# Optimization experiments

Measured on AMD Instinct MI355X. Metric: run time of the kernel, lower is better.

The kernel has to match this reference:

```python
import jax, jax.numpy as jnp
import numpy as np

B, N, K = 4, 4096, 16
C_IN = 128
EPS = 1e-5


def setup_inputs() -> dict:
    key = jax.random.key(0)
    ks = jax.random.split(key, 8)
    c0 = 2 * C_IN + 3  # concat channels: pos_diff(3) + feat2(128) + feat1(128)
    return {
        "pos1": jax.random.normal(ks[0], (B, 3, N), jnp.float32),
        "pos2": jax.random.normal(ks[1], (B, 3, N), jnp.float32),
        "feature1": jax.random.normal(ks[2], (B, C_IN, N), jnp.float32),
        "feature2": jax.random.normal(ks[3], (B, C_IN, N), jnp.float32),
        "W0": jax.random.normal(ks[4], (128, c0), jnp.float32) * 0.05,
        "W1": jax.random.normal(ks[5], (128, 128), jnp.float32) * 0.05,
        "W2": jax.random.normal(ks[6], (128, 128), jnp.float32) * 0.05,
        "g0": jnp.ones((128,), jnp.float32),
        "g1": jnp.ones((128,), jnp.float32),
        "g2": jnp.ones((128,), jnp.float32),
        "b0": jnp.zeros((128,), jnp.float32),
        "b1": jnp.zeros((128,), jnp.float32),
        "b2": jnp.zeros((128,), jnp.float32),
    }


def _knn_idx(pos1, pos2, k):
    # pos1, pos2: (B, 3, N).  For each point in pos1, k nearest points in pos2.
    p1 = pos1.transpose(0, 2, 1)  # (B, N, 3)
    p2 = pos2.transpose(0, 2, 1)  # (B, M, 3)
    d = (jnp.sum(p1 * p1, -1, keepdims=True)
         + jnp.sum(p2 * p2, -1)[:, None, :]
         - 2.0 * jnp.einsum("bnc,bmc->bnm", p1, p2))  # (B, N, M) squared dists
    _, idx = jax.lax.top_k(-d, k)  # (B, N, K)
    return idx


def _group(x, idx):
    # x: (B, C, M), idx: (B, N, K) -> (B, C, N, K)
    xt = x.transpose(0, 2, 1)  # (B, M, C)
    g = jax.vmap(lambda a, i: a[i])(xt, idx)  # (B, N, K, C)
    return g.transpose(0, 3, 1, 2)


def _conv_bn_relu(x, W, g, b):
    # 1x1 conv (no bias) + BatchNorm2d (training: batch stats, biased var) + ReLU
    y = jnp.einsum("oc,bcnk->bonk", W, x)
    mu = jnp.mean(y, axis=(0, 2, 3), keepdims=True)
    var = jnp.var(y, axis=(0, 2, 3), keepdims=True)
    yn = (y - mu) * jax.lax.rsqrt(var + EPS)
    return jax.nn.relu(yn * g[None, :, None, None] + b[None, :, None, None])


def reference(pos1, pos2, feature1, feature2, W0, W1, W2, g0, g1, g2, b0, b1, b2):
    idx = _knn_idx(pos1, pos2, K)                      # (B, N, K)
    pos2_g = _group(pos2, idx)                         # (B, 3, N, K)
    pos_diff = pos2_g - pos1[:, :, :, None]
    feat2_g = _group(feature2, idx)                    # (B, C, N, K)
    feat1_rep = jnp.broadcast_to(feature1[:, :, :, None], (B, C_IN, N, K))
    x = jnp.concatenate([pos_diff, feat2_g, feat1_rep], axis=1)  # (B, 2C+3, N, K)
    x = _conv_bn_relu(x, W0, g0, b0)
    x = _conv_bn_relu(x, W1, g1, b1)
    x = _conv_bn_relu(x, W2, g2, b2)
    feat1_new = jnp.max(x, axis=-1)                    # (B, mlp[-1], N)
    return (pos1, feat1_new)
```

## Files before the change

kernel.cpp:

```cpp
#include <hip/hip_runtime.h>

#define B_ 4
#define N_ 4096
#define K_ 16
#define C_ 128
#define NQ (B_*N_)
#define COLS_TOT (NQ*K_)
#define CNT_F 262144.0f
#define EPS_ 1e-5f

typedef __attribute__((ext_vector_type(8))) short short8;
typedef __attribute__((ext_vector_type(4))) float f4;
typedef __attribute__((ext_vector_type(4))) int i4;

__device__ __forceinline__ unsigned short f2bf(float f){
  unsigned u = __builtin_bit_cast(unsigned, f);
  u = u + 0x7fffu + ((u >> 16) & 1u);
  return (unsigned short)(u >> 16);
}
__device__ __forceinline__ float bf2f(unsigned short h){
  return __builtin_bit_cast(float, ((unsigned)h) << 16);
}
__device__ __forceinline__ int swzc(int c){ return c ^ ((c >> 3) & 7); }

__global__ __launch_bounds__(256) void wconv(
    const float* __restrict__ W0, const float* __restrict__ W1, const float* __restrict__ W2,
    unsigned short* __restrict__ W0b, unsigned short* __restrict__ W0c,
    unsigned short* __restrict__ W1b, unsigned short* __restrict__ W2b)
{
  int i = blockIdx.x * 256 + threadIdx.x;
  int sel = i >> 14, r = i & 16383;
  int o = r >> 7, c = r & 127;
  float v; unsigned short* dst;
  if (sel == 0)      { v = W0[o*259 + 3   + c]; dst = W0b; }
  else if (sel == 1) { v = W0[o*259 + 131 + c]; dst = W0c; }
  else if (sel == 2) { v = W1[o*128 + c];       dst = W1b; }
  else               { v = W2[o*128 + c];       dst = W2b; }
  dst[r] = f2bf(v);
}

__global__ __launch_bounds__(256) void knn_chunk(
    const float* __restrict__ pos1, const float* __restrict__ pos2,
    float* __restrict__ kdout, int* __restrict__ kiout)
{
  __shared__ __align__(16) float pts[1024*4];
  int bx = blockIdx.x;
  int b = bx >> 6, rest = bx & 63, ngrp = rest >> 2, chunk = rest & 3;
  int t = threadIdx.x;
  int m0 = chunk * 1024;
  const float* p2 = pos2 + (size_t)b*3*N_;
  for (int i = 0; i < 4; ++i){
    int m = m0 + i*256 + t;
    float x = p2[m], y = p2[N_ + m], z = p2[2*N_ + m];
    float sq = __fadd_rn(__fadd_rn(__fmul_rn(x,x), __fmul_rn(y,y)), __fmul_rn(z,z));
    f4 v; v.x = x; v.y = y; v.z = z; v.w = sq;
    *(f4*)(pts + (i*256 + t)*4) = v;
  }
  __syncthreads();

  int n = ngrp*256 + t;
  const float* p1 = pos1 + (size_t)b*3*N_;
  float qx = p1[n], qy = p1[N_ + n], qz = p1[2*N_ + n];
  float qs = __fadd_rn(__fadd_rn(__fmul_rn(qx,qx), __fmul_rn(qy,qy)), __fmul_rn(qz,qz));

  float kd[16]; int ki[16];
  #pragma unroll
  for (int j = 0; j < 16; ++j){ kd[j] = 3.4e38f; ki[j] = 0; }
  float worst = 3.4e38f;
  float pd = 0.f; int pi = 0; bool pv = false;

  auto flush = [&](){
    float d0 = pv ? pd : 3.4e38f; int i0 = pi;
    #pragma unroll
    for (int j = 15; j >= 1; --j){
      bool cj = kd[j] > d0, cm = kd[j-1] > d0;
      kd[j] = cj ? (cm ? kd[j-1] : d0) : kd[j];
      ki[j] = cj ? (cm ? ki[j-1] : i0) : ki[j];
    }
    { bool c0 = kd[0] > d0; kd[0] = c0 ? d0 : kd[0]; ki[0] = c0 ? i0 : ki[0]; }
    worst = kd[15]; pv = false;
  };

  for (int it = 0; it < 1024; ++it){
    f4 c = *(const f4*)(pts + it*4);
    float dot = __builtin_fmaf(qz, c.z,
                  __builtin_fmaf(qy, c.y, __fmul_rn(qx, c.x)));
    float d = __fsub_rn(__fadd_rn(qs, c.w), __fmul_rn(2.0f, dot));
    bool pass = d < worst;
    if (__any(pass && pv)) flush();
    if (pass){ pd = d; pi = m0 + it; pv = true; }
    if ((it & 7) == 7){ if (__any(pv)) flush(); }
  }
  if (__any(pv)) flush();

  int q = b*N_ + n;
  #pragma unroll
  for (int j = 0; j < 16; ++j){
    kdout[(size_t)q*64 + chunk*16 + j] = kd[j];
    kiout[(size_t)q*64 + chunk*16 + j] = ki[j];
  }
}

__global__ __launch_bounds__(256) void knn_merge(
    const float* __restrict__ kdin, const int* __restrict__ kiin, int* __restrict__ idxout)
{
  int q = blockIdx.x*256 + threadIdx.x;
  float kd[16]; int ki[16];
  #pragma unroll
  for (int j = 0; j < 16; ++j){ kd[j] = 3.4e38f; ki[j] = 0; }
  const float* dsrc = kdin + (size_t)q*64;
  const int*   isrc = kiin + (size_t)q*64;
  for (int s4 = 0; s4 < 16; ++s4){
    f4 dv = *(const f4*)(dsrc + s4*4);
    i4 iv = *(const i4*)(isrc + s4*4);
    #pragma unroll
    for (int e = 0; e < 4; ++e){
      float d0 = dv[e]; int i0 = iv[e];
      #pragma unroll
      for (int j = 15; j >= 1; --j){
        bool cj = kd[j] > d0, cm = kd[j-1] > d0;
        kd[j] = cj ? (cm ? kd[j-1] : d0) : kd[j];
        ki[j] = cj ? (cm ? ki[j-1] : i0) : ki[j];
      }
      { bool c0 = kd[0] > d0; kd[0] = c0 ? d0 : kd[0]; ki[0] = c0 ? i0 : ki[0]; }
    }
  }
  #pragma unroll
  for (int j = 0; j < 16; ++j) idxout[(size_t)q*16 + j] = ki[j];
}

__global__ __launch_bounds__(256) void p1_gemm(
    const float* __restrict__ feat2, const float* __restrict__ feat1,
    const unsigned short* __restrict__ W0b, const unsigned short* __restrict__ W0c,
    float* __restrict__ F2t, float* __restrict__ PREt)
{
  __shared__ __align__(16) unsigned short X[16*128*8];
  int bid = blockIdx.x;
  int sel = bid >> 7;
  const float* src = sel ? feat1 : feat2;
  const unsigned short* W = sel ? W0c : W0b;
  float* dst = sel ? PREt : F2t;
  int c0 = (bid & 127) * 128;
  int b = c0 >> 12, mm0 = c0 & 4095;
  int t = threadIdx.x;
  {
    int ch = t >> 1, half = t & 1;
    const float* s = src + ((size_t)b*C_ + ch)*N_ + mm0 + half*64;
    int kb = ch >> 3, e = ch & 7;
    for (int mi = 0; mi < 64; ++mi){
      int col = half*64 + mi;
      X[kb*1024 + swzc(col)*8 + e] = f2bf(s[mi]);
    }
  }
  int lane = t & 63, w = t >> 6;
  int or0 = (w >> 1)*64, c0w = (w & 1)*64;
  int lr = lane & 15, lg = lane >> 4;
  short8 af[4][4];
  #pragma unroll
  for (int ks = 0; ks < 4; ++ks)
    #pragma unroll
    for (int i = 0; i < 4; ++i)
      af[ks][i] = *(const short8*)(W + (or0 + 16*i + lr)*128 + ks*32 + 8*lg);
  __syncthreads();

  f4 acc[4][4] = {};
  #pragma unroll
  for (int ks = 0; ks < 4; ++ks){
    short8 bfr[4];
    #pragma unroll
    for (int j = 0; j < 4; ++j)
      bfr[j] = *(const short8*)(X + (ks*4 + lg)*1024 + swzc(c0w + 16*j + lr)*8);
    #pragma unroll
    for (int i = 0; i < 4; ++i)
      #pragma unroll
      for (int j = 0; j < 4; ++j)
        acc[i][j] = __builtin_amdgcn_mfma_f32_16x16x32_bf16(af[ks][i], bfr[j], acc[i][j], 0, 0, 0);
  }
  #pragma unroll
  for (int i = 0; i < 4; ++i)
    #pragma unroll
    for (int j = 0; j < 4; ++j){
      int col = c0 + c0w + 16*j + lr;
      *(f4*)(dst + (size_t)col*C_ + or0 + 16*i + 4*lg) = acc[i][j];
    }
}

__global__ __launch_bounds__(256) void k3_y0(
    const float* __restrict__ pos1, const float* __restrict__ pos2,
    const float* __restrict__ W0, const int* __restrict__ idx,
    const float* __restrict__ F2t, const float* __restrict__ PREt,
    unsigned short* __restrict__ ybuf, float* __restrict__ partials)
{
  __shared__ float w0a[384];
  __shared__ float ldsS[256];
  int t = threadIdx.x;
  for (int i = t; i < 384; i += 256) w0a[i] = W0[(i/3)*259 + (i%3)];
  __syncthreads();
  int cloc = t & 15, chg = t >> 4, ch0 = chg*8;
  float wx[8], wy[8], wz[8];
  #pragma unroll
  for (int e = 0; e < 8; ++e){
    wx[e] = w0a[(ch0+e)*3]; wy[e] = w0a[(ch0+e)*3+1]; wz[e] = w0a[(ch0+e)*3+2];
  }
  float s1[8] = {}, s2[8] = {};
  int base = blockIdx.x * 256;
  for (int it = 0; it < 16; ++it){
    int col = base + it*16 + cloc;
    int nabs = col >> 4;
    int b = nabs >> 12, n = nabs & 4095;
    int m = idx[col];
    float dx = pos2[(size_t)(b*3+0)*N_ + m] - pos1[(size_t)(b*3+0)*N_ + n];
    float dy = pos2[(size_t)(b*3+1)*N_ + m] - pos1[(size_t)(b*3+1)*N_ + n];
    float dz = pos2[(size_t)(b*3+2)*N_ + m] - pos1[(size_t)(b*3+2)*N_ + n];
    const float* f2 = F2t  + ((size_t)b*N_ + m)*C_ + ch0;
    const float* pr = PREt + ((size_t)b*N_ + n)*C_ + ch0;
    short8 sv;
    #pragma unroll
    for (int e = 0; e < 8; ++e){
      float y = f2[e] + pr[e];
      y = fmaf(wx[e], dx, y); y = fmaf(wy[e], dy, y); y = fmaf(wz[e], dz, y);
      s1[e] += y; s2[e] = fmaf(y, y, s2[e]);
      sv[e] = (short)f2bf(y);
    }
    *(short8*)(ybuf + (size_t)col*C_ + ch0) = sv;
  }
  #pragma unroll
  for (int e = 0; e < 8; ++e){
    float a = s1[e], q = s2[e];
    #pragma unroll
    for (int sft = 1; sft < 16; sft <<= 1){ a += __shfl_xor(a, sft); q += __shfl_xor(q, sft); }
    if (cloc == 0){ ldsS[ch0 + e] = a; ldsS[128 + ch0 + e] = q; }
  }
  __syncthreads();
  partials[(size_t)blockIdx.x*256 + t] = ldsS[t];
}

__global__ __launch_bounds__(256) void reduce1(const float* __restrict__ partials,
                                               float* __restrict__ partial2)
{
  int t = threadIdx.x, r0 = blockIdx.x*32;
  float a = 0.f;
  #pragma unroll 4
  for (int i = 0; i < 32; ++i) a += partials[(size_t)(r0+i)*256 + t];
  partial2[(size_t)blockIdx.x*256 + t] = a;
}

__global__ __launch_bounds__(256) void finalize(const float* __restrict__ partial2, int rows,
    const float* __restrict__ g, const float* __restrict__ bb,
    float* __restrict__ cA, float* __restrict__ cB)
{
  __shared__ float sh[256];
  int t = threadIdx.x;
  float a = 0.f;
  for (int i = 0; i < rows; ++i) a += partial2[(size_t)i*256 + t];
  sh[t] = a;
  __syncthreads();
  if (t < 128){
    float mu = sh[t] / CNT_F;
    float var = sh[128 + t] / CNT_F - mu*mu;
    float A = g[t] * rsqrtf(var + EPS_);
    cA[t] = A; cB[t] = bb[t] - mu*A;
  }
}

template<int LAST>
__global__ __launch_bounds__(256,2) void layer_gemm(
    unsigned short* ybuf,
    const unsigned short* __restrict__ Wbf,
    const float* __restrict__ cA, const float* __restrict__ cB,
    float* __restrict__ y2max,
    float* __restrict__ partials)
{
  __shared__ __align__(16) char lds[38912];
  unsigned short* X = (unsigned short*)lds;
  float* ldsA = (float*)(lds + 34816);
  float* ldsB = ldsA + 128;
  float* ldsS = ldsB + 128;
  int t = threadIdx.x;
  int c0 = blockIdx.x * 128;
  if (t < 128){ ldsA[t] = cA[t]; ldsB[t] = cB[t]; }
  ldsS[t] = 0.f; ldsS[256 + t] = 0.f;

  int lane = t & 63, w = t >> 6;
  int or0 = (w >> 1)*64, c0w = (w & 1)*64;
  int lr = lane & 15, lg = lane >> 4;
  short8 af[4][4];
  #pragma unroll
  for (int ks = 0; ks < 4; ++ks)
    #pragma unroll
    for (int i = 0; i < 4; ++i)
      af[ks][i] = *(const short8*)(Wbf + (or0 + 16*i + lr)*128 + ks*32 + 8*lg);
  __syncthreads();

  {
    int colL = t >> 1, half = t & 1;
    const unsigned short* src = ybuf + (size_t)(c0 + colL)*128 + half*64;
    int sc = swzc(colL);
    #pragma unroll
    for (int cc = 0; cc < 8; ++cc){
      int ch0 = half*64 + cc*8;
      short8 yv = *(const short8*)(src + cc*8);
      short8 xv;
      #pragma unroll
      for (int e = 0; e < 8; ++e){
        float f = bf2f((unsigned short)yv[e]);
        float v = fmaf(f, ldsA[ch0 + e], ldsB[ch0 + e]);
        v = v > 0.f ? v : 0.f;
        xv[e] = (short)f2bf(v);
      }
      *(short8*)(X + (ch0 >> 3)*1024 + sc*8) = xv;
    }
  }
  __syncthreads();

  f4 acc[4][4] = {};
  #pragma unroll
  for (int ks = 0; ks < 4; ++ks){
    short8 bfr[4];
    #pragma unroll
    for (int j = 0; j < 4; ++j)
      bfr[j] = *(const short8*)(X + (ks*4 + lg)*1024 + swzc(c0w + 16*j + lr)*8);
    #pragma unroll
    for (int i = 0; i < 4; ++i)
      #pragma unroll
      for (int j = 0; j < 4; ++j)
        acc[i][j] = __builtin_amdgcn_mfma_f32_16x16x32_bf16(af[ks][i], bfr[j], acc[i][j], 0, 0, 0);
  }

  #pragma unroll
  for (int i = 0; i < 4; ++i)
    #pragma unroll
    for (int e = 0; e < 4; ++e){
      float a0 = acc[i][0][e], a1 = acc[i][1][e], a2 = acc[i][2][e], a3 = acc[i][3][e];
      float s1 = (a0 + a1) + (a2 + a3);
      float s2 = (a0*a0 + a1*a1) + (a2*a2 + a3*a3);
      #pragma unroll
      for (int sft = 1; sft < 16; sft <<= 1){ s1 += __shfl_xor(s1, sft); s2 += __shfl_xor(s2, sft); }
      if (lr == 0){
        int o = or0 + 16*i + 4*lg + e;
        ldsS[(w & 1)*256 + o] = s1;
        ldsS[(w & 1)*256 + 128 + o] = s2;
      }
    }

  if (!LAST){
    __syncthreads();
    unsigned short* OT = (unsigned short*)lds;
    #pragma unroll
    for (int i = 0; i < 4; ++i)
      #pragma unroll
      for (int j = 0; j < 4; ++j){
        int col = c0w + 16*j + lr;
        int o0 = or0 + 16*i + 4*lg;
        unsigned long long pv =
            (unsigned long long)f2bf(acc[i][j][0])
          | ((unsigned long long)f2bf(acc[i][j][1]) << 16)
          | ((unsigned long long)f2bf(acc[i][j][2]) << 32)
          | ((unsigned long long)f2bf(acc[i][j][3]) << 48);
        *(unsigned long long*)(OT + col*136 + o0) = pv;
      }
    __syncthreads();
    {
      int colL = t >> 1, half = t & 1;
      unsigned short* dst = ybuf + (size_t)(c0 + colL)*128 + half*64;
      #pragma unroll
      for (int cc = 0; cc < 8; ++cc){
        short8 v = *(const short8*)(OT + colL*136 + half*64 + cc*8);
        *(short8*)(dst + cc*8) = v;
      }
    }
    __syncthreads();
    partials[(size_t)blockIdx.x*256 + t] = ldsS[t] + ldsS[256 + t];
  } else {
    float keep[4][4] = {};
    #pragma unroll
    for (int j = 0; j < 4; ++j)
      #pragma unroll
      for (int i = 0; i < 4; ++i)
        #pragma unroll
        for (int e = 0; e < 4; ++e){
          float v = acc[i][j][e];
          #pragma unroll
          for (int sft = 1; sft < 16; sft <<= 1) v = fmaxf(v, __shfl_xor(v, sft));
          if (lr == j) keep[i][e] = v;
        }
    if (lr < 4){
      int colg = c0 + c0w + 16*lr;
      int nabs = colg >> 4;
      float* dst = y2max + (size_t)nabs*C_;
      #pragma unroll
      for (int i = 0; i < 4; ++i){
        f4 v; v.x = keep[i][0]; v.y = keep[i][1]; v.z = keep[i][2]; v.w = keep[i][3];
        *(f4*)(dst + or0 + 16*i + 4*lg) = v;
      }
    }
    __syncthreads();
    partials[(size_t)blockIdx.x*256 + t] = ldsS[t] + ldsS[256 + t];
  }
}

__global__ __launch_bounds__(256) void k7_out(
    const float* __restrict__ y2max, const float* __restrict__ cA,
    const float* __restrict__ cB, float* __restrict__ outF)
{
  __shared__ __align__(16) float T[128*65];
  int t = threadIdx.x, bid = blockIdx.x;
  int b = bid >> 6, n0 = (bid & 63)*64;
  {
    int nl = t >> 2, o0 = (t & 3)*32;
    const float* src = y2max + ((size_t)b*N_ + n0 + nl)*C_ + o0;
    #pragma unroll
    for (int jj = 0; jj < 8; ++jj){
      f4 v = *(const f4*)(src + jj*4);
      T[(o0 + jj*4 + 0)*65 + nl] = v.x;
      T[(o0 + jj*4 + 1)*65 + nl] = v.y;
      T[(o0 + jj*4 + 2)*65 + nl] = v.z;
      T[(o0 + jj*4 + 3)*65 + nl] = v.w;
    }
  }
  __syncthreads();
  {
    int o = t >> 1, half = t & 1;
    float A = cA[o], Bb = cB[o];
    float* dst = outF + ((size_t)b*C_ + o)*N_ + n0 + half*32;
    #pragma unroll
    for (int jj = 0; jj < 8; ++jj){
      f4 v;
      float x0 = fmaf(T[o*65 + half*32 + jj*4+0], A, Bb);
      float x1 = fmaf(T[o*65 + half*32 + jj*4+1], A, Bb);
      float x2 = fmaf(T[o*65 + half*32 + jj*4+2], A, Bb);
      float x3 = fmaf(T[o*65 + half*32 + jj*4+3], A, Bb);
      v.x = x0 > 0.f ? x0 : 0.f; v.y = x1 > 0.f ? x1 : 0.f;
      v.z = x2 > 0.f ? x2 : 0.f; v.w = x3 > 0.f ? x3 : 0.f;
      *(f4*)(dst + jj*4) = v;
    }
  }
}

extern "C" void kernel_launch(void* const* d_in, const int* in_sizes, int n_in,
                              void* d_out, int out_size, void* d_ws, size_t ws_size,
                              hipStream_t stream)
{
  (void)in_sizes; (void)n_in; (void)out_size; (void)ws_size;
  const float* pos1  = (const float*)d_in[0];
  const float* pos2  = (const float*)d_in[1];
  const float* feat1 = (const float*)d_in[2];
  const float* feat2 = (const float*)d_in[3];
  const float* W0 = (const float*)d_in[4];
  const float* W1 = (const float*)d_in[5];
  const float* W2 = (const float*)d_in[6];
  const float* g0 = (const float*)d_in[7];
  const float* g1 = (const float*)d_in[8];
  const float* g2 = (const float*)d_in[9];
  const float* b0 = (const float*)d_in[10];
  const float* b1 = (const float*)d_in[11];
  const float* b2 = (const float*)d_in[12];

  char* ws = (char*)d_ws;
  size_t off = 0;
  auto alloc = [&](size_t bytes){ size_t r = off; off += (bytes + 255) & ~(size_t)255; return r; };
  float* knn_d   = (float*)(ws + alloc((size_t)NQ*64*4));
  int*   knn_i   = (int*)  (ws + alloc((size_t)NQ*64*4));
  int*   idx     = (int*)  (ws + alloc((size_t)COLS_TOT*4));
  float* F2t     = (float*)(ws + alloc((size_t)NQ*C_*4));
  float* PREt    = (float*)(ws + alloc((size_t)NQ*C_*4));
  unsigned short* ybuf = (unsigned short*)(ws + alloc((size_t)COLS_TOT*C_*2));
  float* y2max   = (float*)(ws + alloc((size_t)NQ*C_*4));
  float* partials= (float*)(ws + alloc((size_t)2048*256*4));
  float* partial2= (float*)(ws + alloc((size_t)64*256*4));
  float* coef    = (float*)(ws + alloc((size_t)6*128*4));
  unsigned short* W0bb = (unsigned short*)(ws + alloc(16384*2));
  unsigned short* W0cb = (unsigned short*)(ws + alloc(16384*2));
  unsigned short* W1b  = (unsigned short*)(ws + alloc(16384*2));
  unsigned short* W2b  = (unsigned short*)(ws + alloc(16384*2));

  float* cA0 = coef,       *cB0 = coef + 128;
  float* cA1 = coef + 256, *cB1 = coef + 384;
  float* cA2 = coef + 512, *cB2 = coef + 640;

  wconv<<<256, 256, 0, stream>>>(W0, W1, W2, W0bb, W0cb, W1b, W2b);
  knn_chunk<<<256, 256, 0, stream>>>(pos1, pos2, knn_d, knn_i);
  knn_merge<<<64, 256, 0, stream>>>(knn_d, knn_i, idx);
  p1_gemm<<<256, 256, 0, stream>>>(feat2, feat1, W0bb, W0cb, F2t, PREt);
  k3_y0<<<1024, 256, 0, stream>>>(pos1, pos2, W0, idx, F2t, PREt, ybuf, partials);
  reduce1<<<32, 256, 0, stream>>>(partials, partial2);
  finalize<<<1, 256, 0, stream>>>(partial2, 32, g0, b0, cA0, cB0);
  layer_gemm<0><<<2048, 256, 0, stream>>>(ybuf, W1b, cA0, cB0, nullptr, partials);
  reduce1<<<64, 256, 0, stream>>>(partials, partial2);
  finalize<<<1, 256, 0, stream>>>(partial2, 64, g1, b1, cA1, cB1);
  layer_gemm<1><<<2048, 256, 0, stream>>>(ybuf, W2b, cA1, cB1, y2max, partials);
  reduce1<<<64, 256, 0, stream>>>(partials, partial2);
  finalize<<<1, 256, 0, stream>>>(partial2, 64, g2, b2, cA2, cB2);
  k7_out<<<256, 256, 0, stream>>>(y2max, cA2, cB2, (float*)d_out + (size_t)B_*3*N_);
  hipMemcpyAsync(d_out, d_in[0], (size_t)B_*3*N_*4, hipMemcpyDeviceToDevice, stream);
}
```

Measured before the change: 414.3 us.

## Split KNN search into 16 chunks per query with early-exit merge

```diff
diff --git a/kernel.cpp b/kernel.cpp
--- a/kernel.cpp
+++ b/kernel.cpp
@@ -43,18 +43,18 @@
     const float* __restrict__ pos1, const float* __restrict__ pos2,
     float* __restrict__ kdout, int* __restrict__ kiout)
 {
-  __shared__ __align__(16) float pts[1024*4];
+  __shared__ __align__(16) float pts[256*4];
   int bx = blockIdx.x;
-  int b = bx >> 6, rest = bx & 63, ngrp = rest >> 2, chunk = rest & 3;
+  int b = bx >> 8, rest = bx & 255, ngrp = rest >> 4, chunk = rest & 15;
   int t = threadIdx.x;
-  int m0 = chunk * 1024;
+  int m0 = chunk * 256;
   const float* p2 = pos2 + (size_t)b*3*N_;
-  for (int i = 0; i < 4; ++i){
-    int m = m0 + i*256 + t;
+  {
+    int m = m0 + t;
     float x = p2[m], y = p2[N_ + m], z = p2[2*N_ + m];
     float sq = __fadd_rn(__fadd_rn(__fmul_rn(x,x), __fmul_rn(y,y)), __fmul_rn(z,z));
     f4 v; v.x = x; v.y = y; v.z = z; v.w = sq;
-    *(f4*)(pts + (i*256 + t)*4) = v;
+    *(f4*)(pts + t*4) = v;
   }
   __syncthreads();
 
@@ -81,23 +81,27 @@
     worst = kd[15]; pv = false;
   };
 
-  for (int it = 0; it < 1024; ++it){
-    f4 c = *(const f4*)(pts + it*4);
-    float dot = __builtin_fmaf(qz, c.z,
-                  __builtin_fmaf(qy, c.y, __fmul_rn(qx, c.x)));
-    float d = __fsub_rn(__fadd_rn(qs, c.w), __fmul_rn(2.0f, dot));
-    bool pass = d < worst;
-    if (__any(pass && pv)) flush();
-    if (pass){ pd = d; pi = m0 + it; pv = true; }
-    if ((it & 7) == 7){ if (__any(pv)) flush(); }
+  for (int bt = 0; bt < 32; ++bt){
+    #pragma unroll
+    for (int e = 0; e < 8; ++e){
+      int it = bt*8 + e;
+      f4 c = *(const f4*)(pts + it*4);
+      float dot = __builtin_fmaf(qz, c.z,
+                    __builtin_fmaf(qy, c.y, __fmul_rn(qx, c.x)));
+      float d = __fsub_rn(__fadd_rn(qs, c.w), __fmul_rn(2.0f, dot));
+      bool pass = d < worst;
+      if (__any(pass && pv)) flush();
+      if (pass){ pd = d; pi = m0 + it; pv = true; }
+    }
+    if (__any(pv)) flush();
   }
   if (__any(pv)) flush();
 
   int q = b*N_ + n;
   #pragma unroll
   for (int j = 0; j < 16; ++j){
-    kdout[(size_t)q*64 + chunk*16 + j] = kd[j];
-    kiout[(size_t)q*64 + chunk*16 + j] = ki[j];
+    kdout[(size_t)q*256 + chunk*16 + j] = kd[j];
+    kiout[(size_t)q*256 + chunk*16 + j] = ki[j];
   }
 }
 
@@ -108,21 +112,30 @@
   float kd[16]; int ki[16];
   #pragma unroll
   for (int j = 0; j < 16; ++j){ kd[j] = 3.4e38f; ki[j] = 0; }
-  const float* dsrc = kdin + (size_t)q*64;
-  const int*   isrc = kiin + (size_t)q*64;
-  for (int s4 = 0; s4 < 16; ++s4){
-    f4 dv = *(const f4*)(dsrc + s4*4);
-    i4 iv = *(const i4*)(isrc + s4*4);
-    #pragma unroll
-    for (int e = 0; e < 4; ++e){
-      float d0 = dv[e]; int i0 = iv[e];
-      #pragma unroll
-      for (int j = 15; j >= 1; --j){
-        bool cj = kd[j] > d0, cm = kd[j-1] > d0;
-        kd[j] = cj ? (cm ? kd[j-1] : d0) : kd[j];
-        ki[j] = cj ? (cm ? ki[j-1] : i0) : ki[j];
+  const float* dsrc = kdin + (size_t)q*256;
+  const int*   isrc = kiin + (size_t)q*256;
+  for (int l = 0; l < 16; ++l){
+    bool dead = false;
+    #pragma unroll 1
+    for (int s4 = 0; s4 < 4; ++s4){
+      if (__all(dead)) break;
+      f4 dv = *(const f4*)(dsrc + l*16 + s4*4);
+      i4 iv = *(const i4*)(isrc + l*16 + s4*4);
+      #pragma unroll
+      for (int e = 0; e < 4; ++e){
+        float d0 = dv[e]; int i0 = iv[e];
+        bool ins = !dead && (kd[15] > d0);
+        dead = dead || !ins;
+        if (ins){
+          #pragma unroll
+          for (int j = 15; j >= 1; --j){
+            bool cj = kd[j] > d0, cm = kd[j-1] > d0;
+            kd[j] = cj ? (cm ? kd[j-1] : d0) : kd[j];
+            ki[j] = cj ? (cm ? ki[j-1] : i0) : ki[j];
+          }
+          bool c0 = kd[0] > d0; kd[0] = c0 ? d0 : kd[0]; ki[0] = c0 ? i0 : ki[0];
+        }
       }
-      { bool c0 = kd[0] > d0; kd[0] = c0 ? d0 : kd[0]; ki[0] = c0 ? i0 : ki[0]; }
     }
   }
   #pragma unroll
@@ -459,8 +472,6 @@
   char* ws = (char*)d_ws;
   size_t off = 0;
   auto alloc = [&](size_t bytes){ size_t r = off; off += (bytes + 255) & ~(size_t)255; return r; };
-  float* knn_d   = (float*)(ws + alloc((size_t)NQ*64*4));
-  int*   knn_i   = (int*)  (ws + alloc((size_t)NQ*64*4));
   int*   idx     = (int*)  (ws + alloc((size_t)COLS_TOT*4));
   float* F2t     = (float*)(ws + alloc((size_t)NQ*C_*4));
   float* PREt    = (float*)(ws + alloc((size_t)NQ*C_*4));
@@ -474,12 +485,15 @@
   unsigned short* W1b  = (unsigned short*)(ws + alloc(16384*2));
   unsigned short* W2b  = (unsigned short*)(ws + alloc(16384*2));
 
+  float* knn_d = (float*)ybuf;
+  int*   knn_i = (int*)((char*)ybuf + (size_t)NQ*256*4);
+
   float* cA0 = coef,       *cB0 = coef + 128;
   float* cA1 = coef + 256, *cB1 = coef + 384;
   float* cA2 = coef + 512, *cB2 = coef + 640;
 
   wconv<<<256, 256, 0, stream>>>(W0, W1, W2, W0bb, W0cb, W1b, W2b);
-  knn_chunk<<<256, 256, 0, stream>>>(pos1, pos2, knn_d, knn_i);
+  knn_chunk<<<1024, 256, 0, stream>>>(pos1, pos2, knn_d, knn_i);
   knn_merge<<<64, 256, 0, stream>>>(knn_d, knn_i, idx);
   p1_gemm<<<256, 256, 0, stream>>>(feat2, feat1, W0bb, W0cb, F2t, PREt);
   k3_y0<<<1024, 256, 0, stream>>>(pos1, pos2, W0, idx, F2t, PREt, ybuf, partials);
```

New measurement: 410.4 us. Within noise of the previous version (-0.9%).
